# Kernel tuning notes

Hardware: AMD Instinct MI355X
Metric: run time of the kernel (lower is better)

## Reference

```python
import jax, jax.numpy as jnp
import numpy as np

N = 10000      # atoms
E = 160000     # edges (avg degree 16)
H = 64         # hidden_channels
R = 64         # num_rbf
MAXZ = 100
RC = 4.5       # cutoff_upper (cutoff_lower = 0)
LN_EPS = 1e-5


def setup_inputs() -> dict:
    key = jax.random.key(0)
    ks = jax.random.split(key, 20)
    z = jax.random.randint(ks[0], (N,), 0, MAXZ, dtype=jnp.int32)
    edge_index = jax.random.randint(ks[1], (2, E), 0, N, dtype=jnp.int32)
    edge_weight = jax.random.uniform(ks[2], (E,), dtype=jnp.float32) * RC
    v = jax.random.normal(ks[3], (E, 3), dtype=jnp.float32)
    edge_vec_norm = v / jnp.linalg.norm(v, axis=-1, keepdims=True)
    edge_attr = jax.random.normal(ks[4], (E, R), dtype=jnp.float32)
    p = lambda k, shape: (jax.random.normal(k, shape, dtype=jnp.float32) * 0.1)
    return {
        'z': z, 'edge_index': edge_index, 'edge_weight': edge_weight,
        'edge_vec_norm': edge_vec_norm, 'edge_attr': edge_attr,
        'emb': p(ks[5], (MAXZ, H)),
        'emb2_w': p(ks[6], (H, 2 * H)), 'emb2_b': p(ks[7], (H,)),
        'dp1_w': p(ks[8], (H, R)), 'dp1_b': p(ks[9], (H,)),
        'dp2_w': p(ks[10], (H, R)), 'dp2_b': p(ks[11], (H,)),
        'dp3_w': p(ks[12], (H, R)), 'dp3_b': p(ks[13], (H,)),
        'ln_g': jnp.ones((H,), jnp.float32), 'ln_b': jnp.zeros((H,), jnp.float32),
        'w1': p(ks[14], (2 * H, H)), 'b1': jnp.zeros((2 * H,), jnp.float32),
        'w2': p(ks[15], (3 * H, 2 * H)), 'b2': jnp.zeros((3 * H,), jnp.float32),
        'm0': p(ks[16], (H, H)), 'm1': p(ks[17], (H, H)), 'm2': p(ks[18], (H, H)),
    }


def reference(z, edge_index, edge_weight, edge_vec_norm, edge_attr,
              emb, emb2_w, emb2_b, dp1_w, dp1_b, dp2_w, dp2_b, dp3_w, dp3_b,
              ln_g, ln_b, w1, b1, w2, b2, m0, m1, m2):
    n_atoms = z.shape[0]
    hc = emb.shape[1]
    src, dst = edge_index[0], edge_index[1]

    # atomic number message Z_ij: concat(Z_i, Z_j) -> Linear  [E,H]
    Zn = emb[z]
    Zij = jnp.concatenate([Zn[src], Zn[dst]], axis=-1) @ emb2_w.T + emb2_b

    # cosine cutoff (cutoff_lower == 0)
    C = 0.5 * (jnp.cos(edge_weight * jnp.pi / RC) + 1.0) * (edge_weight < RC)

    # RBF-gated per-edge channel weights, all [E,H]
    g1 = (edge_attr @ dp1_w.T + dp1_b) * C[:, None] * Zij
    g2 = (edge_attr @ dp2_w.T + dp2_b) * C[:, None] * Zij
    g3 = (edge_attr @ dp3_w.T + dp3_b) * C[:, None] * Zij

    eye = jnp.eye(3, dtype=Zij.dtype)
    vx, vy, vz = edge_vec_norm[:, 0], edge_vec_norm[:, 1], edge_vec_norm[:, 2]
    zero = jnp.zeros_like(vx)
    skew = jnp.stack([zero, -vz, vy, vz, zero, -vx, -vy, vx, zero], axis=-1).reshape(-1, 3, 3)
    outer = edge_vec_norm[:, :, None] * edge_vec_norm[:, None, :]  # [E,3,3], symmetric
    sym = outer - (jnp.trace(outer, axis1=-2, axis2=-1) / 3.0)[:, None, None] * eye

    # per-edge messages [E,H,3,3]
    Iij = g1[:, :, None, None] * eye
    Aij = g2[:, :, None, None] * skew[:, None, :, :]
    Sij = g3[:, :, None, None] * sym[:, None, :, :]

    # scatter-add to atoms
    I = jax.ops.segment_sum(Iij, src, num_segments=n_atoms)
    A = jax.ops.segment_sum(Aij, src, num_segments=n_atoms)
    S = jax.ops.segment_sum(Sij, src, num_segments=n_atoms)

    # tensor norm -> layernorm -> MLP1
    tn = ((I + A + S) ** 2).sum((-2, -1))  # [N,H]
    mu = tn.mean(-1, keepdims=True)
    var = ((tn - mu) ** 2).mean(-1, keepdims=True)
    norm = (tn - mu) / jnp.sqrt(var + LN_EPS) * ln_g + ln_b
    norm = jax.nn.silu(norm @ w1.T + b1)
    norm = jax.nn.silu(norm @ w2.T + b2)
    norm = norm.reshape(-1, hc, 3)
    n0 = norm[..., 0][:, :, None, None]

    # channel-mixing; NOTE: original code applies MLP2[1]/MLP2[2] to the
    # updated I and gates all three with norm[...,0] -- replicated faithfully.
    I = jnp.einsum('nhij,kh->nkij', I, m0) * n0
    A = jnp.einsum('nhij,kh->nkij', I, m1) * n0
    S = jnp.einsum('nhij,kh->nkij', I, m2) * n0
    return I + A + S
```

## Files before the change

kernel.cpp:

```cpp
#include <hip/hip_runtime.h>
#include <stdint.h>

#define NATOMS 10000
#define NEDGES 160000
#define RCUT   4.5f
#define CAP    64
#define ATGRID 1024

#define T_BYTES    ((size_t)NATOMS * 640 * 4)
#define CNT_OFF    (T_BYTES)
#define CNT_BYTES  ((size_t)NATOMS * 4)
#define REC_OFF    (CNT_OFF + CNT_BYTES)
#define REC_BYTES  ((size_t)NATOMS * CAP * 16)
#define EMB_OFF    (REC_OFF + REC_BYTES)
#define EMB_BYTES  ((size_t)100 * 64 * 2)

typedef unsigned short u16;
typedef __bf16 bf16x8 __attribute__((ext_vector_type(8)));
typedef float  f32x4  __attribute__((ext_vector_type(4)));

#define MFMA16(a,b,c) __builtin_amdgcn_mfma_f32_16x16x32_bf16((a),(b),(c),0,0,0)
#define BFMAGIC 0x3F803F80u
#define MSK 0xffff0000u

__device__ __forceinline__ float uf(unsigned int u){ return __uint_as_float(u); }
__device__ __forceinline__ float b2f(u16 u){
  union { unsigned int i; float f; } v; v.i = ((unsigned int)u) << 16; return v.f;
}
__device__ __forceinline__ u16 f2b(float f){
  union { unsigned int i; float f; } v; v.f = f;
  unsigned int b = v.i + 0x7fffu + ((v.i >> 16) & 1u);
  return (u16)(b >> 16);
}
__device__ __forceinline__ float ldf(const void* p, int i, int bf){
  if (bf) return b2f(((const u16*)p)[i]);
  return ((const float*)p)[i];
}
__device__ __forceinline__ bf16x8 ld8bf(const void* p, int i, int bf){
  if (bf) return *(const bf16x8*)((const u16*)p + i);
  const float4* q = (const float4*)((const float*)p + i);
  float4 a = q[0], b = q[1];
  bf16x8 r;
  r[0]=(__bf16)a.x; r[1]=(__bf16)a.y; r[2]=(__bf16)a.z; r[3]=(__bf16)a.w;
  r[4]=(__bf16)b.x; r[5]=(__bf16)b.y; r[6]=(__bf16)b.z; r[7]=(__bf16)b.w;
  return r;
}
__device__ __forceinline__ uint4 ld8pk(const void* p, int i, int bf){
  if (bf) return *(const uint4*)((const u16*)p + i);
  const float4* q = (const float4*)((const float*)p + i);
  float4 a = q[0], b = q[1];
  uint4 r;
  r.x = (unsigned int)f2b(a.x) | ((unsigned int)f2b(a.y) << 16);
  r.y = (unsigned int)f2b(a.z) | ((unsigned int)f2b(a.w) << 16);
  r.z = (unsigned int)f2b(b.x) | ((unsigned int)f2b(b.y) << 16);
  r.w = (unsigned int)f2b(b.z) | ((unsigned int)f2b(b.w) << 16);
  return r;
}
__device__ __forceinline__ void ld8f(const void* p, int i, float* o, int bf){
  if (bf){
    uint4 v = *(const uint4*)((const u16*)p + i);
    o[0]=uf(v.x<<16); o[1]=uf(v.x&MSK); o[2]=uf(v.y<<16); o[3]=uf(v.y&MSK);
    o[4]=uf(v.z<<16); o[5]=uf(v.z&MSK); o[6]=uf(v.w<<16); o[7]=uf(v.w&MSK);
    return;
  }
  const float4* q = (const float4*)((const float*)p + i);
  float4 a = q[0], b = q[1];
  o[0]=a.x; o[1]=a.y; o[2]=a.z; o[3]=a.w; o[4]=b.x; o[5]=b.y; o[6]=b.z; o[7]=b.w;
}
__device__ __forceinline__ uint4 pk8(const float* f){
  uint4 r;
  r.x = (unsigned int)f2b(f[0]) | ((unsigned int)f2b(f[1]) << 16);
  r.y = (unsigned int)f2b(f[2]) | ((unsigned int)f2b(f[3]) << 16);
  r.z = (unsigned int)f2b(f[4]) | ((unsigned int)f2b(f[5]) << 16);
  r.w = (unsigned int)f2b(f[6]) | ((unsigned int)f2b(f[7]) << 16);
  return r;
}

__global__ __launch_bounds__(256) void scatter_kernel(const int* __restrict__ ei,
                                                      const int* __restrict__ z,
                                                      const void* __restrict__ ew,
                                                      const void* __restrict__ evn,
                                                      const void* __restrict__ emb,
                                                      u16* __restrict__ emb16,
                                                      int* __restrict__ cnt,
                                                      uint4* __restrict__ REC,
                                                      const unsigned int* __restrict__ lng){
  const int bf = (lng[0] == BFMAGIC);
  int e = blockIdx.x * 256 + threadIdx.x;
  if (e < 6400) emb16[e] = bf ? ((const u16*)emb)[e] : f2b(((const float*)emb)[e]);
  int s = ei[e], d = ei[NEDGES + e];
  int p = atomicAdd(&cnt[s], 1);
  const float w  = ldf(ew, e, bf);
  const float Cv = (w < RCUT) ? 0.5f*(__cosf(w * (3.14159265358979f / RCUT)) + 1.0f) : 0.0f;
  uint4 rec;
  rec.x = (unsigned int)e;
  rec.y = (unsigned int)z[d];
  rec.z = (unsigned int)f2b(ldf(evn, 3*e + 0, bf)) | ((unsigned int)f2b(ldf(evn, 3*e + 1, bf)) << 16);
  rec.w = (unsigned int)f2b(ldf(evn, 3*e + 2, bf)) | ((unsigned int)f2b(Cv) << 16);
  if (p < CAP) REC[(size_t)s*CAP + p] = rec;
}

__global__ __launch_bounds__(256)
void atomT_kernel(
    const int* __restrict__ z,
    const u16* __restrict__ emb16,
    const void* __restrict__ attr,
    const uint4* __restrict__ REC,
    const int* __restrict__ cnt,
    const void* __restrict__ e2w, const void* __restrict__ e2b,
    const void* __restrict__ d1w, const void* __restrict__ d1b,
    const void* __restrict__ d2w, const void* __restrict__ d2b,
    const void* __restrict__ d3w, const void* __restrict__ d3b,
    float* __restrict__ T,
    const unsigned int* __restrict__ lng)
{
  __shared__ __align__(16) u16 dpW[3][64][64];
  __shared__ __align__(16) u16 e2W[64][128];

  const int bf  = (lng[0] == BFMAGIC);
  const int tid = threadIdx.x;
  const void* dps[3] = {d1w, d2w, d3w};
  for (int idx = tid; idx < 1536; idx += 256){
    int w = idx >> 9, rem = idx & 511, r = rem >> 3, c8 = rem & 7;
    *(bf16x8*)&dpW[w][r][(c8 ^ (r & 7))*8] = ld8bf(dps[w], r*64 + c8*8, bf);
  }
  for (int idx = tid; idx < 1024; idx += 256){
    int r = idx >> 4, c8 = idx & 15;
    *(bf16x8*)&e2W[r][(c8 ^ (r & 7))*8] = ld8bf(e2w, r*128 + c8*8, bf);
  }
  __syncthreads();

  const int lane = tid & 63;
  const int wave = tid >> 6;
  const int hh   = lane & 15;
  const int quad = lane >> 4;
  const int half = wave & 1;
  const int ntb  = half * 2;
  const int wpair = wave >> 1;

  float be2[2], bd1[2], bd2[2], bd3[2];
#pragma unroll
  for (int j = 0; j < 2; j++){
    int h = hh + 16*(ntb + j);
    be2[j] = ldf(e2b, h, bf); bd1[j] = ldf(d1b, h, bf);
    bd2[j] = ldf(d2b, h, bf); bd3[j] = ldf(d3b, h, bf);
  }

  const int NPAIR = NATOMS / 2;
  const unsigned EMAX = (unsigned)(NEDGES - 1);

  int pr  = blockIdx.x;
  int n   = pr * 2 + wpair;
  int cnA = cnt[n];
  int zA  = z[n];

  int prB    = pr + ATGRID;
  bool moreB = (prB < NPAIR);
  int nB     = moreB ? (prB * 2 + wpair) : n;
  int cnB    = cnt[nB];
  int zB     = z[nB];

  int e0 = n * CAP;
  int nv = min(cnA, CAP);
  uint4 recA = REC[e0 + min((int)hh, max(nv - 1, 0))];

  bf16x8 af0, af1, zf2, zf3;
  {
    const int ex = (int)min(recA.x, EMAX);
    af0 = ld8bf(attr, ex*64 + quad*8, bf);
    af1 = ld8bf(attr, ex*64 + 32 + quad*8, bf);
    const int ey = (int)min(recA.y, 99u);
    zf2 = *(const bf16x8*)(emb16 + ey*64 + quad*8);
    zf3 = *(const bf16x8*)(emb16 + ey*64 + 32 + quad*8);
  }

  while (true) {
    const int e1 = e0 + nv;

    const int e0B = nB * CAP;
    const int nvB = min(cnB, CAP);
    uint4 recB = REC[e0B + min((int)hh, max(nvB - 1, 0))];

    const int prC   = prB + ATGRID;
    const bool moreC = (prC < NPAIR);
    const int nC    = moreC ? (prC * 2 + wpair) : nB;
    const int cnC   = cnt[nC];
    const int zC    = z[nC];

    bf16x8 zf0 = *(const bf16x8*)(emb16 + zA*64 + quad*8);
    bf16x8 zf1 = *(const bf16x8*)(emb16 + zA*64 + 32 + quad*8);

    float P[10][2];
#pragma unroll
    for (int c = 0; c < 10; c++){ P[c][0] = 0.f; P[c][1] = 0.f; }

    for (int base = e0; base < e1; base += 16){
      const bool lastC = (base + 16 >= e1);
      uint4 recN = REC[min(base + 16 + hh, e1 - 1)];

      f32x4 aZ[2], a1[2], a2[2], a3[2];
#pragma unroll
      for (int j = 0; j < 2; j++){
        aZ[j] = (f32x4){0.f,0.f,0.f,0.f};
        a1[j] = (f32x4){0.f,0.f,0.f,0.f};
        a2[j] = (f32x4){0.f,0.f,0.f,0.f};
        a3[j] = (f32x4){0.f,0.f,0.f,0.f};
      }

#pragma unroll
      for (int j = 0; j < 2; j++){
        const int h  = hh + 16*(ntb + j);
        const int s0 = (quad       ^ (h & 7)) * 8;
        const int s1 = ((quad + 4) ^ (h & 7)) * 8;
        bf16x8 b;
        b = *(const bf16x8*)&dpW[0][h][s0];           a1[j] = MFMA16(af0, b, a1[j]);
        b = *(const bf16x8*)&dpW[0][h][s1];           a1[j] = MFMA16(af1, b, a1[j]);
        b = *(const bf16x8*)&dpW[1][h][s0];           a2[j] = MFMA16(af0, b, a2[j]);
        b = *(const bf16x8*)&dpW[1][h][s1];           a2[j] = MFMA16(af1, b, a2[j]);
        b = *(const bf16x8*)&dpW[2][h][s0];           a3[j] = MFMA16(af0, b, a3[j]);
        b = *(const bf16x8*)&dpW[2][h][s1];           a3[j] = MFMA16(af1, b, a3[j]);
        b = *(const bf16x8*)&e2W[h][s0];              aZ[j] = MFMA16(zf0, b, aZ[j]);
        b = *(const bf16x8*)&e2W[h][s1];              aZ[j] = MFMA16(zf1, b, aZ[j]);
        b = *(const bf16x8*)&e2W[h][((quad + 8)  ^ (h & 7)) * 8];  aZ[j] = MFMA16(zf2, b, aZ[j]);
        b = *(const bf16x8*)&e2W[h][((quad + 12) ^ (h & 7)) * 8];  aZ[j] = MFMA16(zf3, b, aZ[j]);
      }

      bf16x8 afN0, afN1, zfN2, zfN3;
      if (!lastC){
        const int ex = (int)min(recN.x, EMAX);
        afN0 = ld8bf(attr, ex*64 + quad*8, bf);
        afN1 = ld8bf(attr, ex*64 + 32 + quad*8, bf);
        const int ey = (int)min(recN.y, 99u);
        zfN2 = *(const bf16x8*)(emb16 + ey*64 + quad*8);
        zfN3 = *(const bf16x8*)(emb16 + ey*64 + 32 + quad*8);
      }

#pragma unroll
      for (int r = 0; r < 4; r++){
        const int ii = base + quad*4 + r;
        const bool ea = (ii < e1);
        const int srcl = quad*20 + r;
        const unsigned int rz = (unsigned int)__shfl((int)recA.z, srcl, 64);
        const unsigned int rw = (unsigned int)__shfl((int)recA.w, srcl, 64);
        const float Cv = ea ? b2f((u16)(rw >> 16)) : 0.f;
        const float vx = b2f((u16)(rz & 0xffffu));
        const float vy = b2f((u16)(rz >> 16));
        const float vz = b2f((u16)(rw & 0xffffu));
        const float xx = vx*vx - (1.f/3.f), yy = vy*vy - (1.f/3.f), zz = vz*vz - (1.f/3.f);
        const float xy = vx*vy, xz = vx*vz, yz = vy*vz;
#pragma unroll
        for (int j = 0; j < 2; j++){
          const float czv = Cv * (aZ[j][r] + be2[j]);
          const float g1 = (a1[j][r] + bd1[j]) * czv;
          const float g2 = (a2[j][r] + bd2[j]) * czv;
          const float g3 = (a3[j][r] + bd3[j]) * czv;
          P[0][j] += g1;
          P[1][j] += g2*vx; P[2][j] += g2*vy; P[3][j] += g2*vz;
          P[4][j] += g3*xx; P[5][j] += g3*yy; P[6][j] += g3*zz;
          P[7][j] += g3*xy; P[8][j] += g3*xz; P[9][j] += g3*yz;
        }
      }

      if (!lastC){ recA = recN; af0 = afN0; af1 = afN1; zf2 = zfN2; zf3 = zfN3; }
    }

    {
      const int ex = (int)min(recB.x, EMAX);
      af0 = ld8bf(attr, ex*64 + quad*8, bf);
      af1 = ld8bf(attr, ex*64 + 32 + quad*8, bf);
      const int ey = (int)min(recB.y, 99u);
      zf2 = *(const bf16x8*)(emb16 + ey*64 + quad*8);
      zf3 = *(const bf16x8*)(emb16 + ey*64 + 32 + quad*8);
    }

#pragma unroll
    for (int c = 0; c < 10; c++)
#pragma unroll
      for (int j = 0; j < 2; j++){
        float v = P[c][j];
        v += __shfl_xor(v, 16, 64);
        v += __shfl_xor(v, 32, 64);
        P[c][j] = v;
      }

    if ((quad >> 1) == half){
      float* Tn = T + (size_t)n * 640;
#pragma unroll
      for (int c = 0; c < 10; c++)
        Tn[c*64 + lane] = P[c][quad & 1];
    }

    if (!moreB) break;
    pr = prB; n = nB; zA = zB; e0 = e0B; nv = nvB; recA = recB;
    prB = prC; moreB = moreC; nB = nC; cnB = cnC; zB = zC;
  }
}

__global__ __launch_bounds__(256) void mlp_kernel(
    const float* __restrict__ T,
    const void* __restrict__ ln_g, const void* __restrict__ ln_b,
    const void* __restrict__ w1,  const void* __restrict__ b1,
    const void* __restrict__ w2,  const void* __restrict__ b2p,
    const void* __restrict__ m0,  const void* __restrict__ m1,
    const void* __restrict__ m2,  void* __restrict__ out,
    const unsigned int* __restrict__ lng)
{
  __shared__ __align__(16) u16 w1L[128][72];
  __shared__ __align__(16) u16 w2L[64][136];
  __shared__ __align__(16) u16 m0L[64][72];
  __shared__ __align__(16) u16 msL[64][72];
  __shared__ __align__(16) float xbuf[4][64];
  __shared__ __align__(16) float hbuf2[4][128];
  __shared__ __align__(16) float isoB[4][64];
  __shared__ __align__(16) float i1B[4][64];

  const int bf  = (lng[0] == BFMAGIC);
  const int tid = threadIdx.x;

  for (int idx = tid; idx < 1024; idx += 256){
    int r = idx >> 3, c8 = idx & 7;
    *(uint4*)&w1L[r][c8*8] = ld8pk(w1, r*64 + c8*8, bf);
  }
  for (int idx = tid; idx < 1024; idx += 256){
    int r = idx >> 4, c8 = idx & 15;
    *(uint4*)&w2L[r][c8*8] = ld8pk(w2, (3*r)*128 + c8*8, bf);
  }
  for (int idx = tid; idx < 512; idx += 256){
    int r = idx >> 3, c8 = idx & 7;
    *(uint4*)&m0L[r][c8*8] = ld8pk(m0, r*64 + c8*8, bf);
    float f[8], g[8];
    ld8f(m1, r*64 + c8*8, f, bf);
    ld8f(m2, r*64 + c8*8, g, bf);
#pragma unroll
    for (int q = 0; q < 8; q++) f[q] += g[q];
    *(uint4*)&msL[r][c8*8] = pk8(f);
  }
  __syncthreads();

  const int wave = tid >> 6;
  const int h    = tid & 63;
  const int wid  = blockIdx.x * 4 + wave;

  const float lngh = ldf(ln_g, h, bf), lnbh = ldf(ln_b, h, bf);
  const float b1a = ldf(b1, h, bf), b1b = ldf(b1, h + 64, bf);
  const float b2h = ldf(b2p, 3*h, bf);

  const uint4*  A4 = (const uint4*)&w1L[h][0];
  const uint4*  B4 = (const uint4*)&w1L[h + 64][0];
  const uint4*  W4 = (const uint4*)&w2L[h][0];
  const uint4*  M4 = (const uint4*)&m0L[h][0];
  const uint4*  S4 = (const uint4*)&msL[h][0];
  const float4* X4  = (const float4*)&xbuf[wave][0];
  const float4* H4  = (const float4*)&hbuf2[wave][0];
  const float4* I4  = (const float4*)&isoB[wave][0];
  const float4* J4  = (const float4*)&i1B[wave][0];

  const int NITER = (NATOMS + 2047) / 2048;
  for (int it = 0; it < NITER; it++){
    const int n   = wid + it * 2048;
    const bool act = (n < NATOMS);
    const int na  = act ? n : 0;

    const float* Tn = T + (size_t)na * 640;
    const float iso = Tn[h];
    const float wx = Tn[64+h], wy = Tn[128+h], wz = Tn[192+h];
    const float sxx = Tn[256+h], syy = Tn[320+h], szz = Tn[384+h];
    const float sxy = Tn[448+h], sxz = Tn[512+h], syz = Tn[576+h];
    const float tn = (iso+sxx)*(iso+sxx) + (iso+syy)*(iso+syy) + (iso+szz)*(iso+szz)
                   + 2.f*(sxy*sxy + sxz*sxz + syz*syz + wx*wx + wy*wy + wz*wz);
    isoB[wave][h] = iso;

    float s = tn;
#pragma unroll
    for (int off = 32; off; off >>= 1) s += __shfl_xor(s, off, 64);
    const float mu = s * (1.f/64.f);
    const float d0 = tn - mu;
    float v = d0 * d0;
#pragma unroll
    for (int off = 32; off; off >>= 1) v += __shfl_xor(v, off, 64);
    v *= (1.f/64.f);
    xbuf[wave][h] = d0 * rsqrtf(v + 1e-5f) * lngh + lnbh;
    __syncthreads();

    float acc0 = b1a, acc1 = b1b;
#pragma unroll
    for (int q = 0; q < 8; q++){
      const uint4 A = A4[q], B = B4[q];
      const float4 x0 = X4[2*q], x1 = X4[2*q + 1];
      acc0 += uf(A.x << 16)*x0.x + uf(A.x & MSK)*x0.y;
      acc0 += uf(A.y << 16)*x0.z + uf(A.y & MSK)*x0.w;
      acc0 += uf(A.z << 16)*x1.x + uf(A.z & MSK)*x1.y;
      acc0 += uf(A.w << 16)*x1.z + uf(A.w & MSK)*x1.w;
      acc1 += uf(B.x << 16)*x0.x + uf(B.x & MSK)*x0.y;
      acc1 += uf(B.y << 16)*x0.z + uf(B.y & MSK)*x0.w;
      acc1 += uf(B.z << 16)*x1.x + uf(B.z & MSK)*x1.y;
      acc1 += uf(B.w << 16)*x1.z + uf(B.w & MSK)*x1.w;
    }
    acc0 = acc0 / (1.f + __expf(-acc0));
    acc1 = acc1 / (1.f + __expf(-acc1));
    hbuf2[wave][h] = acc0; hbuf2[wave][h + 64] = acc1;
    __syncthreads();

    float acc2 = b2h, t1 = 0.f;
#pragma unroll
    for (int q = 0; q < 16; q++){
      const uint4 W = W4[q];
      const float4 y0 = H4[2*q], y1 = H4[2*q + 1];
      acc2 += uf(W.x << 16)*y0.x + uf(W.x & MSK)*y0.y;
      acc2 += uf(W.y << 16)*y0.z + uf(W.y & MSK)*y0.w;
      acc2 += uf(W.z << 16)*y1.x + uf(W.z & MSK)*y1.y;
      acc2 += uf(W.w << 16)*y1.z + uf(W.w & MSK)*y1.w;
    }
#pragma unroll
    for (int q = 0; q < 8; q++){
      const uint4 M = M4[q];
      const float4 x0 = I4[2*q], x1 = I4[2*q + 1];
      t1 += uf(M.x << 16)*x0.x + uf(M.x & MSK)*x0.y;
      t1 += uf(M.y << 16)*x0.z + uf(M.y & MSK)*x0.w;
      t1 += uf(M.z << 16)*x1.x + uf(M.z & MSK)*x1.y;
      t1 += uf(M.w << 16)*x1.z + uf(M.w & MSK)*x1.w;
    }
    const float n0 = acc2 / (1.f + __expf(-acc2));
    const float iso1 = t1 * n0;
    i1B[wave][h] = iso1;
    __syncthreads();

    float t23 = 0.f;
#pragma unroll
    for (int q = 0; q < 8; q++){
      const uint4 M = S4[q];
      const float4 x0 = J4[2*q], x1 = J4[2*q + 1];
      t23 += uf(M.x << 16)*x0.x + uf(M.x & MSK)*x0.y;
      t23 += uf(M.y << 16)*x0.z + uf(M.y & MSK)*x0.w;
      t23 += uf(M.z << 16)*x1.x + uf(M.z & MSK)*x1.y;
      t23 += uf(M.w << 16)*x1.z + uf(M.w & MSK)*x1.w;
    }
    const float dval = iso1 + t23 * n0;

    if (act){
      if (bf){
        u16* o = (u16*)out + (size_t)n * 576 + h * 9;
        const u16 db = f2b(dval);
        o[0] = db; o[1] = 0; o[2] = 0;
        o[3] = 0;  o[4] = db; o[5] = 0;
        o[6] = 0;  o[7] = 0;  o[8] = db;
      } else {
        float* o = (float*)out + (size_t)n * 576 + h * 9;
        o[0] = dval; o[1] = 0.f; o[2] = 0.f;
        o[3] = 0.f;  o[4] = dval; o[5] = 0.f;
        o[6] = 0.f;  o[7] = 0.f;  o[8] = dval;
      }
    }
    __syncthreads();
  }
}

extern "C" void kernel_launch(void* const* d_in, const int* in_sizes, int n_in,
                              void* d_out, int out_size, void* d_ws, size_t ws_size,
                              hipStream_t stream) {
  const int* z    = (const int*)d_in[0];
  const int* ei   = (const int*)d_in[1];
  const void* ew   = d_in[2];
  const void* evn  = d_in[3];
  const void* attr = d_in[4];
  const void* emb  = d_in[5];
  const void* e2w  = d_in[6];
  const void* e2b  = d_in[7];
  const void* d1w  = d_in[8];
  const void* d1b  = d_in[9];
  const void* d2w  = d_in[10];
  const void* d2b  = d_in[11];
  const void* d3w  = d_in[12];
  const void* d3b  = d_in[13];
  const void* ln_g = d_in[14];
  const void* ln_b = d_in[15];
  const void* w1   = d_in[16];
  const void* b1   = d_in[17];
  const void* w2   = d_in[18];
  const void* b2p  = d_in[19];
  const void* m0   = d_in[20];
  const void* m1   = d_in[21];
  const void* m2   = d_in[22];
  const unsigned int* lng = (const unsigned int*)ln_g;

  char* ws = (char*)d_ws;
  float*   T     = (float*)ws;
  int*     cnt   = (int*)(ws + CNT_OFF);
  uint4*   REC   = (uint4*)(ws + REC_OFF);
  u16*     emb16 = (u16*)(ws + EMB_OFF);

  hipMemsetAsync(cnt, 0, CNT_BYTES, stream);
  scatter_kernel<<<NEDGES/256, 256, 0, stream>>>(ei, z, ew, evn, emb, emb16, cnt, REC, lng);
  atomT_kernel<<<ATGRID, 256, 0, stream>>>(z, emb16, attr, REC, cnt, e2w, e2b,
                                           d1w, d1b, d2w, d2b, d3w, d3b, T, lng);
  mlp_kernel<<<512, 256, 0, stream>>>(T, ln_g, ln_b, w1, b1, w2, b2p,
                                      m0, m1, m2, d_out, lng);
}
```

Before: 277.8 us.

## Assign one atom per block with each wave handling sixteen channels

Before, each block handled a pair of atoms, and each pair of waves split the 64 channels (two 16-channel tiles per wave). Now all four waves work on the same atom, each owning one 16-channel tile. This halves per-wave MFMA work and register pressure per edge chunk and drops the two-ahead prefetch. The cost is that every wave redundantly loads the same edge records, attribute rows and embeddings, and each block processes twice as many atom iterations.

```diff
diff --git a/kernel.cpp b/kernel.cpp
--- a/kernel.cpp
+++ b/kernel.cpp
@@ -134,34 +134,26 @@
   const int wave = tid >> 6;
   const int hh   = lane & 15;
   const int quad = lane >> 4;
-  const int half = wave & 1;
-  const int ntb  = half * 2;
-  const int wpair = wave >> 1;
-
-  float be2[2], bd1[2], bd2[2], bd3[2];
-#pragma unroll
-  for (int j = 0; j < 2; j++){
-    int h = hh + 16*(ntb + j);
-    be2[j] = ldf(e2b, h, bf); bd1[j] = ldf(d1b, h, bf);
-    bd2[j] = ldf(d2b, h, bf); bd3[j] = ldf(d3b, h, bf);
-  }
-
-  const int NPAIR = NATOMS / 2;
+  const int h    = hh + 16*wave;
+
+  const float be2 = ldf(e2b, h, bf);
+  const float bd1 = ldf(d1b, h, bf);
+  const float bd2 = ldf(d2b, h, bf);
+  const float bd3 = ldf(d3b, h, bf);
+
+  const int s0 = (quad        ^ (h & 7)) * 8;
+  const int s1 = ((quad + 4)  ^ (h & 7)) * 8;
+  const int s2 = ((quad + 8)  ^ (h & 7)) * 8;
+  const int s3 = ((quad + 12) ^ (h & 7)) * 8;
+
   const unsigned EMAX = (unsigned)(NEDGES - 1);
 
-  int pr  = blockIdx.x;
-  int n   = pr * 2 + wpair;
-  int cnA = cnt[n];
-  int zA  = z[n];
-
-  int prB    = pr + ATGRID;
-  bool moreB = (prB < NPAIR);
-  int nB     = moreB ? (prB * 2 + wpair) : n;
-  int cnB    = cnt[nB];
-  int zB     = z[nB];
+  int n   = blockIdx.x;
+  int cn  = cnt[n];
+  int zsv = z[n];
 
   int e0 = n * CAP;
-  int nv = min(cnA, CAP);
+  int nv = min(cn, CAP);
   uint4 recA = REC[e0 + min((int)hh, max(nv - 1, 0))];
 
   bf16x8 af0, af1, zf2, zf3;
@@ -177,52 +169,43 @@
   while (true) {
     const int e1 = e0 + nv;
 
-    const int e0B = nB * CAP;
-    const int nvB = min(cnB, CAP);
+    const int nn    = n + ATGRID;
+    const bool more = (nn < NATOMS);
+    const int nnB   = more ? nn : n;
+    const int cnB   = cnt[nnB];
+    const int zB    = z[nnB];
+    const int e0B   = nnB * CAP;
+    const int nvB   = min(cnB, CAP);
     uint4 recB = REC[e0B + min((int)hh, max(nvB - 1, 0))];
 
-    const int prC   = prB + ATGRID;
-    const bool moreC = (prC < NPAIR);
-    const int nC    = moreC ? (prC * 2 + wpair) : nB;
-    const int cnC   = cnt[nC];
-    const int zC    = z[nC];
-
-    bf16x8 zf0 = *(const bf16x8*)(emb16 + zA*64 + quad*8);
-    bf16x8 zf1 = *(const bf16x8*)(emb16 + zA*64 + 32 + quad*8);
-
-    float P[10][2];
-#pragma unroll
-    for (int c = 0; c < 10; c++){ P[c][0] = 0.f; P[c][1] = 0.f; }
+    bf16x8 zf0 = *(const bf16x8*)(emb16 + zsv*64 + quad*8);
+    bf16x8 zf1 = *(const bf16x8*)(emb16 + zsv*64 + 32 + quad*8);
+
+    float P[10];
+#pragma unroll
+    for (int c = 0; c < 10; c++) P[c] = 0.f;
 
     for (int base = e0; base < e1; base += 16){
       const bool lastC = (base + 16 >= e1);
       uint4 recN = REC[min(base + 16 + hh, e1 - 1)];
 
-      f32x4 aZ[2], a1[2], a2[2], a3[2];
-#pragma unroll
-      for (int j = 0; j < 2; j++){
-        aZ[j] = (f32x4){0.f,0.f,0.f,0.f};
-        a1[j] = (f32x4){0.f,0.f,0.f,0.f};
-        a2[j] = (f32x4){0.f,0.f,0.f,0.f};
-        a3[j] = (f32x4){0.f,0.f,0.f,0.f};
-      }
-
-#pragma unroll
-      for (int j = 0; j < 2; j++){
-        const int h  = hh + 16*(ntb + j);
-        const int s0 = (quad       ^ (h & 7)) * 8;
-        const int s1 = ((quad + 4) ^ (h & 7)) * 8;
+      f32x4 aZ = (f32x4){0.f,0.f,0.f,0.f};
+      f32x4 a1 = (f32x4){0.f,0.f,0.f,0.f};
+      f32x4 a2 = (f32x4){0.f,0.f,0.f,0.f};
+      f32x4 a3 = (f32x4){0.f,0.f,0.f,0.f};
+
+      {
         bf16x8 b;
-        b = *(const bf16x8*)&dpW[0][h][s0];           a1[j] = MFMA16(af0, b, a1[j]);
-        b = *(const bf16x8*)&dpW[0][h][s1];           a1[j] = MFMA16(af1, b, a1[j]);
-        b = *(const bf16x8*)&dpW[1][h][s0];           a2[j] = MFMA16(af0, b, a2[j]);
-        b = *(const bf16x8*)&dpW[1][h][s1];           a2[j] = MFMA16(af1, b, a2[j]);
-        b = *(const bf16x8*)&dpW[2][h][s0];           a3[j] = MFMA16(af0, b, a3[j]);
-        b = *(const bf16x8*)&dpW[2][h][s1];           a3[j] = MFMA16(af1, b, a3[j]);
-        b = *(const bf16x8*)&e2W[h][s0];              aZ[j] = MFMA16(zf0, b, aZ[j]);
-        b = *(const bf16x8*)&e2W[h][s1];              aZ[j] = MFMA16(zf1, b, aZ[j]);
-        b = *(const bf16x8*)&e2W[h][((quad + 8)  ^ (h & 7)) * 8];  aZ[j] = MFMA16(zf2, b, aZ[j]);
-        b = *(const bf16x8*)&e2W[h][((quad + 12) ^ (h & 7)) * 8];  aZ[j] = MFMA16(zf3, b, aZ[j]);
+        b = *(const bf16x8*)&dpW[0][h][s0];  a1 = MFMA16(af0, b, a1);
+        b = *(const bf16x8*)&dpW[0][h][s1];  a1 = MFMA16(af1, b, a1);
+        b = *(const bf16x8*)&dpW[1][h][s0];  a2 = MFMA16(af0, b, a2);
+        b = *(const bf16x8*)&dpW[1][h][s1];  a2 = MFMA16(af1, b, a2);
+        b = *(const bf16x8*)&dpW[2][h][s0];  a3 = MFMA16(af0, b, a3);
+        b = *(const bf16x8*)&dpW[2][h][s1];  a3 = MFMA16(af1, b, a3);
+        b = *(const bf16x8*)&e2W[h][s0];     aZ = MFMA16(zf0, b, aZ);
+        b = *(const bf16x8*)&e2W[h][s1];     aZ = MFMA16(zf1, b, aZ);
+        b = *(const bf16x8*)&e2W[h][s2];     aZ = MFMA16(zf2, b, aZ);
+        b = *(const bf16x8*)&e2W[h][s3];     aZ = MFMA16(zf3, b, aZ);
       }
 
       bf16x8 afN0, afN1, zfN2, zfN3;
@@ -248,17 +231,14 @@
         const float vz = b2f((u16)(rw & 0xffffu));
         const float xx = vx*vx - (1.f/3.f), yy = vy*vy - (1.f/3.f), zz = vz*vz - (1.f/3.f);
         const float xy = vx*vy, xz = vx*vz, yz = vy*vz;
-#pragma unroll
-        for (int j = 0; j < 2; j++){
-          const float czv = Cv * (aZ[j][r] + be2[j]);
-          const float g1 = (a1[j][r] + bd1[j]) * czv;
-          const float g2 = (a2[j][r] + bd2[j]) * czv;
-          const float g3 = (a3[j][r] + bd3[j]) * czv;
-          P[0][j] += g1;
-          P[1][j] += g2*vx; P[2][j] += g2*vy; P[3][j] += g2*vz;
-          P[4][j] += g3*xx; P[5][j] += g3*yy; P[6][j] += g3*zz;
-          P[7][j] += g3*xy; P[8][j] += g3*xz; P[9][j] += g3*yz;
-        }
+        const float czv = Cv * (aZ[r] + be2);
+        const float g1 = (a1[r] + bd1) * czv;
+        const float g2 = (a2[r] + bd2) * czv;
+        const float g3 = (a3[r] + bd3) * czv;
+        P[0] += g1;
+        P[1] += g2*vx; P[2] += g2*vy; P[3] += g2*vz;
+        P[4] += g3*xx; P[5] += g3*yy; P[6] += g3*zz;
+        P[7] += g3*xy; P[8] += g3*xz; P[9] += g3*yz;
       }
 
       if (!lastC){ recA = recN; af0 = afN0; af1 = afN1; zf2 = zfN2; zf3 = zfN3; }
@@ -274,25 +254,22 @@
     }
 
 #pragma unroll
-    for (int c = 0; c < 10; c++)
-#pragma unroll
-      for (int j = 0; j < 2; j++){
-        float v = P[c][j];
-        v += __shfl_xor(v, 16, 64);
-        v += __shfl_xor(v, 32, 64);
-        P[c][j] = v;
-      }
-
-    if ((quad >> 1) == half){
-      float* Tn = T + (size_t)n * 640;
+    for (int c = 0; c < 10; c++){
+      float v = P[c];
+      v += __shfl_xor(v, 16, 64);
+      v += __shfl_xor(v, 32, 64);
+      P[c] = v;
+    }
+
+    if (quad == 0){
+      float* Tn = T + (size_t)n * 640 + 16*wave + hh;
 #pragma unroll
       for (int c = 0; c < 10; c++)
-        Tn[c*64 + lane] = P[c][quad & 1];
-    }
-
-    if (!moreB) break;
-    pr = prB; n = nB; zA = zB; e0 = e0B; nv = nvB; recA = recB;
-    prB = prC; moreB = moreC; nB = nC; cnB = cnC; zB = zC;
+        Tn[c*64] = P[c];
+    }
+
+    if (!more) break;
+    n = nn; cn = cnB; zsv = zB; e0 = e0B; nv = nvB; recA = recB;
   }
 }
 
```

Measured after the change: 245.4 us. 1.13x faster.
